# Performance work log

Measured on AMD Instinct MI355X. Metric: run time of the kernel, lower is better.

## Reference

```python
import jax, jax.numpy as jnp
import numpy as np

N_NODES = 50000
N_EDGES = 800000
F_IN = 128
HID = 32
H_IN = 4
N_CLS = 47
H_OUT = 4
NEG_SLOPE = 0.2


def _param(k, shape, scale=0.1):
    return jax.random.normal(k, shape, dtype=jnp.float32) * scale


def setup_inputs() -> dict:
    key = jax.random.key(0)
    ks = jax.random.split(key, 14)
    return {
        "x": jax.random.normal(ks[0], (N_NODES, F_IN), dtype=jnp.float32),
        "edge_index": jax.random.randint(ks[1], (2, N_EDGES), 0, N_NODES, dtype=jnp.int64),
        # layer 1: in -> hidden, heads_in, concat
        "W1": _param(ks[2], (F_IN, H_IN * HID)),
        "a1s": _param(ks[3], (H_IN, HID)),
        "a1d": _param(ks[4], (H_IN, HID)),
        "b1": _param(ks[5], (H_IN * HID,)),
        # layer 2: hidden*heads -> hidden, heads_in, concat
        "W2": _param(ks[6], (H_IN * HID, H_IN * HID)),
        "a2s": _param(ks[7], (H_IN, HID)),
        "a2d": _param(ks[8], (H_IN, HID)),
        "b2": _param(ks[9], (H_IN * HID,)),
        # layer 3: hidden*heads -> out, heads_out, mean (concat=False)
        "W3": _param(ks[10], (H_IN * HID, H_OUT * N_CLS)),
        "a3s": _param(ks[11], (H_OUT, N_CLS)),
        "a3d": _param(ks[12], (H_OUT, N_CLS)),
        "b3": _param(ks[13], (N_CLS,)),
    }


def gat_conv(x, W, att_src, att_dst, bias, src, dst, concat):
    """PyG GATConv (self-loops pre-appended in src/dst, eval mode)."""
    n = x.shape[0]
    H, C = att_src.shape
    h = (x @ W).reshape(n, H, C)                      # [N, H, C]
    a_src = jnp.sum(h * att_src[None], axis=-1)       # [N, H]
    a_dst = jnp.sum(h * att_dst[None], axis=-1)       # [N, H]
    alpha = a_src[src] + a_dst[dst]                   # [E, H]
    alpha = jnp.where(alpha >= 0, alpha, NEG_SLOPE * alpha)
    # segment softmax over destination nodes
    m = jax.ops.segment_max(alpha, dst, num_segments=n)  # [N, H]
    e = jnp.exp(alpha - m[dst])
    denom = jax.ops.segment_sum(e, dst, num_segments=n)  # [N, H]
    w = e / denom[dst]                                   # [E, H]
    msg = h[src] * w[:, :, None]                         # [E, H, C]
    out = jax.ops.segment_sum(msg, dst, num_segments=n)  # [N, H, C]
    if concat:
        out = out.reshape(n, H * C)
    else:
        out = out.mean(axis=1)
    return out + bias


def reference(x, edge_index, W1, a1s, a1d, b1, W2, a2s, a2d, b2, W3, a3s, a3d, b3):
    n = x.shape[0]
    loops = jnp.arange(n, dtype=edge_index.dtype)
    src = jnp.concatenate([edge_index[0], loops])
    dst = jnp.concatenate([edge_index[1], loops])
    h = gat_conv(x, W1, a1s, a1d, b1, src, dst, concat=True)
    h = jax.nn.relu(h)
    h = gat_conv(h, W2, a2s, a2d, b2, src, dst, concat=True)
    h = jax.nn.relu(h)
    h = gat_conv(h, W3, a3s, a3d, b3, src, dst, concat=False)
    return jax.nn.log_softmax(h, axis=1)
```

## Files before the change

### kernel.cpp

```cpp
#include <hip/hip_runtime.h>

typedef unsigned short u16;
typedef unsigned int uint32;
typedef __attribute__((ext_vector_type(8))) short short8;
typedef __attribute__((ext_vector_type(4))) float float4v;

#define N_NODES 50000
#define N_EDGES 800000
#define N_TOT   850000
#define SCAN_BLOCKS ((N_NODES + 255) / 256)
#define NBH 256
#define NB_BKT ((N_NODES + 255) >> 8)

__device__ __forceinline__ float b2f(u16 u) {
  return __uint_as_float(((unsigned int)u) << 16);
}
__device__ __forceinline__ u16 f2b(float f) {
  unsigned int x = __float_as_uint(f);
  unsigned int r = (x + 0x7fffu + ((x >> 16) & 1u)) >> 16;
  return (u16)r;
}
__device__ __forceinline__ float lo_bf(uint32 g) { return __uint_as_float(g << 16); }
__device__ __forceinline__ float hi_bf(uint32 g) { return __uint_as_float(g & 0xffff0000u); }
__device__ __forceinline__ u16 conv_elem(const void* src, int i, int isf32) {
  if (isf32) return f2b(((const float*)src)[i]);
  return ((const u16*)src)[i];
}
__device__ __forceinline__ float lrelu(float a) { return (a >= 0.f) ? a : 0.2f * a; }
__device__ __forceinline__ int eget(const int* __restrict__ ei, int i, int isI64) {
  return isI64 ? ei[2 * i] : ei[i];
}

__global__ void detect_mode(const u16* __restrict__ x16, const int* __restrict__ ei32,
                            int* __restrict__ flags) {
  __shared__ int sh_f32, sh_i32;
  int tid = threadIdx.x;
  if (tid == 0) { sh_f32 = 0; sh_i32 = 0; }
  __syncthreads();
  int emax = 0;
  for (int i = tid; i < 4096; i += 256) {
    int e = (x16[i] >> 7) & 0xFF;
    emax = emax > e ? emax : e;
  }
  if (emax >= 140) atomicOr(&sh_f32, 1);
  if (ei32[2 * tid + 1] != 0) atomicOr(&sh_i32, 1);
  __syncthreads();
  if (tid == 0) { flags[0] = sh_f32; flags[1] = sh_i32 ? 0 : 1; }
}

__global__ void convert_x4(const void* __restrict__ x, const int* __restrict__ flags,
                           u16* __restrict__ out, int n4) {
  int i = blockIdx.x * blockDim.x + threadIdx.x;
  if (i >= n4) return;
  if (flags[0]) {
    float4 v = ((const float4*)x)[i];
    ushort4 o;
    o.x = f2b(v.x); o.y = f2b(v.y); o.z = f2b(v.z); o.w = f2b(v.w);
    ((ushort4*)out)[i] = o;
  } else {
    ((ushort4*)out)[i] = ((const ushort4*)x)[i];
  }
}

__global__ void reorder_all(const void* W1, const void* W2, const void* W3,
                            const void* a1s, const void* a1d, const void* b1,
                            const void* a2s, const void* a2d, const void* b2,
                            const void* a3s, const void* a3d, const void* b3,
                            const int* __restrict__ flags,
                            u16* __restrict__ Wf1, u16* __restrict__ Wf2,
                            u16* __restrict__ Wf3, u16* __restrict__ wt) {
  int idx = blockIdx.x * blockDim.x + threadIdx.x;
  int f32 = flags[0];
  if (idx < 57344) {
    const void* W; u16* Wf; int NCOLS, li;
    if (idx < 16384)      { W = W1; Wf = Wf1; NCOLS = 128; li = idx; }
    else if (idx < 32768) { W = W2; Wf = Wf2; NCOLS = 128; li = idx - 16384; }
    else                  { W = W3; Wf = Wf3; NCOLS = 188; li = idx - 32768; }
    int j = li & 7;
    int l = (li >> 3) & 63;
    int c = (li >> 9) & 3;
    int t = li >> 11;
    int k = c * 32 + (l >> 4) * 8 + j;
    int n = t * 16 + (l & 15);
    Wf[li] = (n < NCOLS) ? conv_elem(W, k * NCOLS + n, f32) : (u16)0;
  } else {
    int li = idx - 57344;
    const void* src; int off;
    if (li < 128)       { src = a1s; off = 16384; }
    else if (li < 256)  { src = a1d; off = 16512; li -= 128; }
    else if (li < 384)  { src = b1;  off = 16640; li -= 256; }
    else if (li < 512)  { src = a2s; off = 33152; li -= 384; }
    else if (li < 640)  { src = a2d; off = 33280; li -= 512; }
    else if (li < 768)  { src = b2;  off = 33408; li -= 640; }
    else if (li < 956)  { src = a3s; off = 57600; li -= 768; }
    else if (li < 1144) { src = a3d; off = 57788; li -= 956; }
    else if (li < 1191) { src = b3;  off = 57976; li -= 1144; }
    else return;
    wt[off + li] = conv_elem(src, li, f32);
  }
}


__global__ __launch_bounds__(256) void pack_hist(const int* __restrict__ ei,
                                                 const int* __restrict__ flags,
                                                 uint32* __restrict__ epack,
                                                 int* __restrict__ cnt, int nE) {
  __shared__ int hist[NB_BKT];
  for (int t = threadIdx.x; t < NB_BKT; t += 256) hist[t] = 0;
  __syncthreads();
  const int i64 = flags[1];
  const int chunk = (nE + NBH - 1) / NBH;
  const int lo = blockIdx.x * chunk;
  const int hi = min(lo + chunk, nE);
  for (int e = lo + (int)threadIdx.x; e < hi; e += 256) {
    int s = eget(ei, e, i64);
    int d = eget(ei, nE + e, i64);
    epack[e] = ((uint32)d << 16) | (uint32)s;
    atomicAdd(&hist[d >> 8], 1);
  }
  __syncthreads();
  for (int t = threadIdx.x; t < NB_BKT; t += 256) cnt[t * NBH + blockIdx.x] = hist[t];
}

__global__ __launch_bounds__(256) void scan_cols(int* __restrict__ cnt,
                                                 int* __restrict__ total) {
  __shared__ int ws[4];
  const int bkt = blockIdx.x;
  const int tid = threadIdx.x, lane = tid & 63, wv = tid >> 6;
  int v = cnt[bkt * NBH + tid];
  int incl = v;
#pragma unroll
  for (int off = 1; off < 64; off <<= 1) {
    int t = __shfl_up(incl, off, 64);
    if (lane >= off) incl += t;
  }
  if (lane == 63) ws[wv] = incl;
  __syncthreads();
  if (tid == 0) {
    int s = 0;
#pragma unroll
    for (int w = 0; w < 4; w++) { int t = ws[w]; ws[w] = s; s += t; }
    total[bkt] = s;
  }
  __syncthreads();
  cnt[bkt * NBH + tid] = ws[wv] + incl - v;
}

__global__ __launch_bounds__(256) void scan_base(const int* __restrict__ total,
                                                 int* __restrict__ base) {
  __shared__ int ws[4];
  const int tid = threadIdx.x, lane = tid & 63, wv = tid >> 6;
  int v = (tid < NB_BKT) ? total[tid] : 0;
  int incl = v;
#pragma unroll
  for (int off = 1; off < 64; off <<= 1) {
    int t = __shfl_up(incl, off, 64);
    if (lane >= off) incl += t;
  }
  if (lane == 63) ws[wv] = incl;
  __syncthreads();
  if (tid == 0) {
    int s = 0;
#pragma unroll
    for (int w = 0; w < 4; w++) { int t = ws[w]; ws[w] = s; s += t; }
    base[NB_BKT] = s;
  }
  __syncthreads();
  if (tid < NB_BKT) base[tid] = ws[wv] + incl - v;
}

__global__ __launch_bounds__(256) void scatter_coarse(const uint32* __restrict__ epack,
                                                      const int* __restrict__ cnt,
                                                      const int* __restrict__ base,
                                                      uint32* __restrict__ staging, int nE) {
  __shared__ int lcur[NB_BKT];
  for (int t = threadIdx.x; t < NB_BKT; t += 256)
    lcur[t] = base[t] + cnt[t * NBH + blockIdx.x];
  __syncthreads();
  const int chunk = (nE + NBH - 1) / NBH;
  const int lo = blockIdx.x * chunk;
  const int hi = min(lo + chunk, nE);
  for (int e = lo + (int)threadIdx.x; e < hi; e += 256) {
    uint32 pk = epack[e];
    int p = atomicAdd(&lcur[pk >> 24], 1);
    staging[p] = pk;
  }
}

__global__ __launch_bounds__(256) void bucket_deg(const uint32* __restrict__ staging,
                                                  const int* __restrict__ base,
                                                  int* __restrict__ deg, int nN) {
  __shared__ int hist[256];
  const int b = blockIdx.x;
  hist[threadIdx.x] = 0;
  __syncthreads();
  const int lo = base[b], hi = base[b + 1];
  for (int i = lo + (int)threadIdx.x; i < hi; i += 256)
    atomicAdd(&hist[(staging[i] >> 16) & 255], 1);
  __syncthreads();
  const int n = (b << 8) + threadIdx.x;
  if (n < nN) deg[n] = hist[threadIdx.x];
}

__global__ __launch_bounds__(256) void scan_blocks(const int* __restrict__ deg,
                                                   int* __restrict__ part,
                                                   int* __restrict__ bsum, int n) {
  __shared__ int ws[4];
  int tid = threadIdx.x;
  int gid = blockIdx.x * 256 + tid;
  int lane = tid & 63, wv = tid >> 6;
  int v = (gid < n) ? (deg[gid] + 1) : 0;
  int incl = v;
#pragma unroll
  for (int off = 1; off < 64; off <<= 1) {
    int t = __shfl_up(incl, off, 64);
    if (lane >= off) incl += t;
  }
  if (lane == 63) ws[wv] = incl;
  __syncthreads();
  if (tid == 0) {
    int s = 0;
#pragma unroll
    for (int w = 0; w < 4; w++) { int t = ws[w]; ws[w] = s; s += t; }
    bsum[blockIdx.x] = s;
  }
  __syncthreads();
  if (gid < n) part[gid] = ws[wv] + incl - v;
}

__global__ __launch_bounds__(256) void scan_bsum(const int* __restrict__ bsum,
                                                 int* __restrict__ boff,
                                                 int* __restrict__ total, int nb) {
  __shared__ int ws[4];
  int tid = threadIdx.x;
  int lane = tid & 63, wv = tid >> 6;
  int v = (tid < nb) ? bsum[tid] : 0;
  int incl = v;
#pragma unroll
  for (int off = 1; off < 64; off <<= 1) {
    int t = __shfl_up(incl, off, 64);
    if (lane >= off) incl += t;
  }
  if (lane == 63) ws[wv] = incl;
  __syncthreads();
  if (tid == 0) {
    int s = 0;
#pragma unroll
    for (int w = 0; w < 4; w++) { int t = ws[w]; ws[w] = s; s += t; }
    *total = s;
  }
  __syncthreads();
  if (tid < nb) boff[tid] = ws[wv] + incl - v;
}

__global__ __launch_bounds__(256) void scan_add(int* __restrict__ row_start,
                                                const int* __restrict__ boff,
                                                const int* __restrict__ deg,
                                                u16* __restrict__ csr_dst,
                                                u16* __restrict__ csr_src,
                                                int* __restrict__ csr_src32, int n) {
  int gid = blockIdx.x * 256 + threadIdx.x;
  if (gid < n) {
    int v = row_start[gid] + boff[blockIdx.x];
    row_start[gid] = v;
    csr_src[v] = (u16)gid;
    csr_src32[v] = gid;
    int cnt = deg[gid] + 1;
    u16 g16 = (u16)gid;
    for (int k = 0; k < cnt; k++) csr_dst[v + k] = g16;
  }
}

__global__ __launch_bounds__(256) void place_csr(const uint32* __restrict__ staging,
                                                 const int* __restrict__ base,
                                                 const int* __restrict__ row_start,
                                                 u16* __restrict__ csr_src16,
                                                 int* __restrict__ csr_src32, int nN) {
  __shared__ int cur[256];
  const int b = blockIdx.x;
  const int n = (b << 8) + threadIdx.x;
  if (n < nN) cur[threadIdx.x] = row_start[n] + 1;
  __syncthreads();
  const int lo = base[b], hi = base[b + 1];
  for (int i = lo + (int)threadIdx.x; i < hi; i += 256) {
    uint32 pk = staging[i];
    int p = atomicAdd(&cur[(pk >> 16) & 255], 1);
    u16 s = (u16)(pk & 0xffffu);
    csr_src16[p] = s;
    csr_src32[p] = (int)s;
  }
}

template <int NT, int NCOLS, int STRIDE, bool FUSE_A, bool CMAJOR, bool FUSE3>
__global__ __launch_bounds__(256) void gemm_mfma(const u16* __restrict__ X,
                                                 const u16* __restrict__ Wf,
                                                 const u16* __restrict__ attS,
                                                 const u16* __restrict__ attD,
                                                 u16* __restrict__ H,
                                                 float* __restrict__ a_s,
                                                 float* __restrict__ a_d, int M) {
  const int wid = __builtin_amdgcn_readfirstlane(threadIdx.x >> 6);
  const int lane = threadIdx.x & 63;
  const int row0 = (blockIdx.x * 4 + wid) * 16;
  if (row0 >= M) return;
  const int qr = lane >> 4;
  const int ln = lane & 15;

  float4v acc[NT];
#pragma unroll
  for (int t = 0; t < NT; t++) acc[t] = (float4v){0.f, 0.f, 0.f, 0.f};

  const short8* Wf8 = (const short8*)Wf;
  const u16* xrow = X + (size_t)(row0 + ln) * 128 + qr * 8;

#pragma unroll
  for (int c = 0; c < 4; c++) {
    short8 afrag = *(const short8*)(xrow + c * 32);
#pragma unroll
    for (int t = 0; t < NT; t++) {
      short8 bfrag = Wf8[(t * 4 + c) * 64 + lane];
      acc[t] = __builtin_amdgcn_mfma_f32_16x16x32_bf16(afrag, bfrag, acc[t], 0, 0, 0);
    }
  }

#pragma unroll
  for (int t = 0; t < NT; t++) {
    int col = t * 16 + ln;
    if (col < NCOLS) {
      int off;
      if constexpr (CMAJOR) {
        int h = (col >= 141) ? 3 : (col >= 94) ? 2 : (col >= 47) ? 1 : 0;
        int c = col - h * 47;
        off = c * 4 + h;
      } else {
        off = col;
      }
#pragma unroll
      for (int i = 0; i < 4; i++) {
        H[(size_t)(row0 + qr * 4 + i) * STRIDE + off] = f2b(acc[t][i]);
      }
    }
  }

  if constexpr (FUSE_A) {
    float aSf[NT], aDf[NT];
#pragma unroll
    for (int t = 0; t < NT; t++) {
      aSf[t] = b2f(attS[t * 16 + ln]);
      aDf[t] = b2f(attD[t * 16 + ln]);
    }
#pragma unroll
    for (int h = 0; h < 4; h++) {
#pragma unroll
      for (int i = 0; i < 4; i++) {
        float s = acc[2 * h][i] * aSf[2 * h] + acc[2 * h + 1][i] * aSf[2 * h + 1];
        float d = acc[2 * h][i] * aDf[2 * h] + acc[2 * h + 1][i] * aDf[2 * h + 1];
#pragma unroll
        for (int m = 1; m < 16; m <<= 1) {
          s += __shfl_xor(s, m, 64);
          d += __shfl_xor(d, m, 64);
        }
        if (ln == 0) {
          int r = row0 + qr * 4 + i;
          a_s[r * 4 + h] = s;
          a_d[r * 4 + h] = d;
        }
      }
    }
  }

  if constexpr (FUSE3) {
    float sh[4][4], dh[4][4];
#pragma unroll
    for (int h = 0; h < 4; h++)
#pragma unroll
      for (int i = 0; i < 4; i++) { sh[h][i] = 0.f; dh[h][i] = 0.f; }
#pragma unroll
    for (int t = 0; t < NT; t++) {
      int col = t * 16 + ln;
      bool v = (col < NCOLS);
      float aS = v ? b2f(attS[col]) : 0.f;
      float aD = v ? b2f(attD[col]) : 0.f;
      int hh = (col >= 141) ? 3 : (col >= 94) ? 2 : (col >= 47) ? 1 : 0;
      float aS0 = (hh == 0) ? aS : 0.f, aS1 = (hh == 1) ? aS : 0.f;
      float aS2 = (hh == 2) ? aS : 0.f, aS3 = (hh == 3) ? aS : 0.f;
      float aD0 = (hh == 0) ? aD : 0.f, aD1 = (hh == 1) ? aD : 0.f;
      float aD2 = (hh == 2) ? aD : 0.f, aD3 = (hh == 3) ? aD : 0.f;
#pragma unroll
      for (int i = 0; i < 4; i++) {
        float a = acc[t][i];
        sh[0][i] += a * aS0; sh[1][i] += a * aS1;
        sh[2][i] += a * aS2; sh[3][i] += a * aS3;
        dh[0][i] += a * aD0; dh[1][i] += a * aD1;
        dh[2][i] += a * aD2; dh[3][i] += a * aD3;
      }
    }
#pragma unroll
    for (int h = 0; h < 4; h++) {
#pragma unroll
      for (int i = 0; i < 4; i++) {
        float s = sh[h][i], d = dh[h][i];
#pragma unroll
        for (int m = 1; m < 16; m <<= 1) {
          s += __shfl_xor(s, m, 64);
          d += __shfl_xor(d, m, 64);
        }
        if (ln == 0) {
          int r = row0 + qr * 4 + i;
          a_s[r * 4 + h] = s;
          a_d[r * 4 + h] = d;
        }
      }
    }
  }
}

__global__ __launch_bounds__(256) void edge_weights(const u16* __restrict__ csr_src,
                                                    const u16* __restrict__ csr_dst,
                                                    const float* __restrict__ a_s,
                                                    const float* __restrict__ a_d,
                                                    uint2* __restrict__ w, int nE) {
  int e = blockIdx.x * blockDim.x + threadIdx.x;
  if (e >= nE) return;
  int s = csr_src[e], d = csr_dst[e];
  float4 as = ((const float4*)a_s)[s];
  float4 ad = ((const float4*)a_d)[d];
  float w0 = __expf(lrelu(as.x + ad.x));
  float w1 = __expf(lrelu(as.y + ad.y));
  float w2 = __expf(lrelu(as.z + ad.z));
  float w3 = __expf(lrelu(as.w + ad.w));
  uint2 o;
  o.x = ((uint32)f2b(w1) << 16) | (uint32)f2b(w0);
  o.y = ((uint32)f2b(w3) << 16) | (uint32)f2b(w2);
  w[e] = o;
}


__global__ __launch_bounds__(256) void aggregate12(const u16* __restrict__ h,
                                                   const u16* __restrict__ wbuf,
                                                   const int* __restrict__ row_start,
                                                   const int* __restrict__ csr_src,
                                                   const u16* __restrict__ bias,
                                                   u16* __restrict__ out, int nN) {
  const int lane = threadIdx.x & 63;
  const int wid = __builtin_amdgcn_readfirstlane(threadIdx.x >> 6);
  const int n = blockIdx.x * 4 + wid;
  if (n >= nN) return;
  const int hL = lane >> 4;
  const uint32* h32 = (const uint32*)h;
  const float bias0 = b2f(bias[2 * lane]);
  const float bias1 = b2f(bias[2 * lane + 1]);
  int beg = row_start[n], end = row_start[n + 1];

  float acc0 = 0.f, acc1 = 0.f, den = 0.f;
  int e = beg;
  for (; e + 3 < end; e += 4) {
    int s[4];
    u16 wv[4];
    uint32 g[4];
#pragma unroll
    for (int j = 0; j < 4; j++) s[j] = csr_src[e + j];
#pragma unroll
    for (int j = 0; j < 4; j++) wv[j] = wbuf[(e + j) * 4 + hL];
#pragma unroll
    for (int j = 0; j < 4; j++) g[j] = h32[s[j] * 64 + lane];
#pragma unroll
    for (int j = 0; j < 4; j++) {
      float w = b2f(wv[j]);
      den += w;
      acc0 += w * lo_bf(g[j]);
      acc1 += w * hi_bf(g[j]);
    }
  }
  for (; e < end; ++e) {
    int s = csr_src[e];
    float w = b2f(wbuf[e * 4 + hL]);
    uint32 g = h32[s * 64 + lane];
    den += w;
    acc0 += w * lo_bf(g);
    acc1 += w * hi_bf(g);
  }
  float inv = 1.0f / den;
  float o0 = fmaxf(acc0 * inv + bias0, 0.f);
  float o1 = fmaxf(acc1 * inv + bias1, 0.f);
  uint32 packed = ((uint32)f2b(o1) << 16) | (uint32)f2b(o0);
  ((uint32*)out)[n * 64 + lane] = packed;
}

__global__ __launch_bounds__(256) void aggregate3(const u16* __restrict__ h3,
                                                  const uint2* __restrict__ wbuf,
                                                  const int* __restrict__ row_start,
                                                  const int* __restrict__ csr_src,
                                                  const u16* __restrict__ b3,
                                                  const int* __restrict__ flags,
                                                  void* __restrict__ out, int nN) {
  const int lane = threadIdx.x & 63;
  const int wid = __builtin_amdgcn_readfirstlane(threadIdx.x >> 6);
  const int n = blockIdx.x * 4 + wid;
  if (n >= nN) return;
  const bool act = lane < 47;
  const int lidx = act ? lane : 0;
  const float b3v = act ? b2f(b3[lane]) : 0.f;
  const int isf32 = flags[0];
  const uint2* h3v = (const uint2*)h3;
  int beg = row_start[n], end = row_start[n + 1];

  float den0 = 0.f, den1 = 0.f, den2 = 0.f, den3 = 0.f;
  float acc0 = 0.f, acc1 = 0.f, acc2 = 0.f, acc3 = 0.f;
  int e = beg;
  for (; e + 3 < end; e += 4) {
    int s[4];
    uint2 wp[4];
    uint2 g[4];
#pragma unroll
    for (int j = 0; j < 4; j++) s[j] = csr_src[e + j];
#pragma unroll
    for (int j = 0; j < 4; j++) wp[j] = wbuf[e + j];
#pragma unroll
    for (int j = 0; j < 4; j++) g[j] = h3v[(size_t)s[j] * 48 + lidx];
#pragma unroll
    for (int j = 0; j < 4; j++) {
      float w0 = lo_bf(wp[j].x), w1 = hi_bf(wp[j].x);
      float w2 = lo_bf(wp[j].y), w3 = hi_bf(wp[j].y);
      den0 += w0; den1 += w1; den2 += w2; den3 += w3;
      acc0 += w0 * lo_bf(g[j].x);
      acc1 += w1 * hi_bf(g[j].x);
      acc2 += w2 * lo_bf(g[j].y);
      acc3 += w3 * hi_bf(g[j].y);
    }
  }
  for (; e < end; ++e) {
    int s = csr_src[e];
    uint2 wp = wbuf[e];
    uint2 g = h3v[(size_t)s * 48 + lidx];
    float w0 = lo_bf(wp.x), w1 = hi_bf(wp.x);
    float w2 = lo_bf(wp.y), w3 = hi_bf(wp.y);
    den0 += w0; den1 += w1; den2 += w2; den3 += w3;
    acc0 += w0 * lo_bf(g.x);
    acc1 += w1 * hi_bf(g.x);
    acc2 += w2 * lo_bf(g.y);
    acc3 += w3 * hi_bf(g.y);
  }
  float val = act ? 0.25f * (acc0 / den0 + acc1 / den1 + acc2 / den2 + acc3 / den3) + b3v
                  : -1e30f;
  float mx = val;
#pragma unroll
  for (int m = 1; m < 64; m <<= 1) mx = fmaxf(mx, __shfl_xor(mx, m, 64));
  float ex = act ? __expf(val - mx) : 0.f;
  float sm = ex;
#pragma unroll
  for (int m = 1; m < 64; m <<= 1) sm += __shfl_xor(sm, m, 64);
  float lse = mx + __logf(sm);
  if (act) {
    float r = val - lse;
    if (isf32) ((float*)out)[n * 47 + lane] = r;
    else       ((u16*)out)[n * 47 + lane] = f2b(r);
  }
}


extern "C" void kernel_launch(void* const* d_in, const int* in_sizes, int n_in,
                              void* d_out, int out_size, void* d_ws, size_t ws_size,
                              hipStream_t stream) {
  const void* x   = d_in[0];
  const void* ei  = d_in[1];
  const void* W1  = d_in[2];
  const void* a1s = d_in[3];
  const void* a1d = d_in[4];
  const void* b1  = d_in[5];
  const void* W2  = d_in[6];
  const void* a2s = d_in[7];
  const void* a2d = d_in[8];
  const void* b2  = d_in[9];
  const void* W3  = d_in[10];
  const void* a3s = d_in[11];
  const void* a3d = d_in[12];
  const void* b3  = d_in[13];
  const int* ei32 = (const int*)ei;

  auto au = [](size_t v) { return (v + 255) & ~(size_t)255; };
  char* p = (char*)d_ws;
  int* flags     = (int*)p; p += 256;
  u16* wt        = (u16*)p; p += au((size_t)58023 * 2);
  u16* Wf1       = (u16*)p; p += au((size_t)16384 * 2);
  u16* Wf2       = (u16*)p; p += au((size_t)16384 * 2);
  u16* Wf3       = (u16*)p; p += au((size_t)24576 * 2);
  int* deg       = (int*)p; p += au((size_t)N_NODES * 4);
  int* row_start = (int*)p; p += au((size_t)(N_NODES + 1) * 4);
  int* cnt       = (int*)p; p += au((size_t)NB_BKT * NBH * 4);
  int* btotal    = (int*)p; p += au((size_t)NB_BKT * 4);
  int* bbase     = (int*)p; p += au((size_t)(NB_BKT + 1) * 4);
  int* bsum      = (int*)p; p += au((size_t)SCAN_BLOCKS * 4);
  int* boff      = (int*)p; p += au((size_t)SCAN_BLOCKS * 4);
  u16* csr_src16 = (u16*)p; p += au((size_t)N_TOT * 2);
  u16* csr_dst   = (u16*)p; p += au((size_t)N_TOT * 2);
  int* csr_src32 = (int*)p; p += au((size_t)N_TOT * 4);
  uint2* wbuf    = (uint2*)p; p += au((size_t)N_TOT * 8);
  float* a_s     = (float*)p; p += au((size_t)N_NODES * 4 * 4);
  float* a_d     = (float*)p; p += au((size_t)N_NODES * 4 * 4);
  u16* x_c       = (u16*)p; p += au((size_t)N_NODES * 128 * 2);
  u16* hA        = (u16*)p; p += au((size_t)N_NODES * 128 * 2);
  u16* h3        = (u16*)p; p += au((size_t)N_NODES * 192 * 2);
  u16* hB        = x_c;
  uint32* epack   = (uint32*)h3;
  uint32* staging = (uint32*)(h3 + 1600000);

  const u16* a1sc = wt + 16384;
  const u16* a1dc = wt + 16512;
  const u16* b1c  = wt + 16640;
  const u16* a2sc = wt + 33152;
  const u16* a2dc = wt + 33280;
  const u16* b2c  = wt + 33408;
  const u16* a3sc = wt + 57600;
  const u16* a3dc = wt + 57788;
  const u16* b3c  = wt + 57976;

  const int nodeBlocks = (N_NODES + 3) / 4;
  const int gemmBlocks = (N_NODES / 16 + 3) / 4;
  const int edgeBlocks = (N_TOT + 255) / 256;

  detect_mode<<<1, 256, 0, stream>>>((const u16*)x, ei32, flags);
  convert_x4<<<(N_NODES * 128 / 4 + 255) / 256, 256, 0, stream>>>(x, flags, x_c,
                                                                  N_NODES * 128 / 4);
  reorder_all<<<229, 256, 0, stream>>>(W1, W2, W3, a1s, a1d, b1, a2s, a2d, b2,
                                       a3s, a3d, b3, flags, Wf1, Wf2, Wf3, wt);

  pack_hist<<<NBH, 256, 0, stream>>>(ei32, flags, epack, cnt, N_EDGES);
  scan_cols<<<NB_BKT, 256, 0, stream>>>(cnt, btotal);
  scan_base<<<1, 256, 0, stream>>>(btotal, bbase);
  scatter_coarse<<<NBH, 256, 0, stream>>>(epack, cnt, bbase, staging, N_EDGES);
  bucket_deg<<<NB_BKT, 256, 0, stream>>>(staging, bbase, deg, N_NODES);
  scan_blocks<<<SCAN_BLOCKS, 256, 0, stream>>>(deg, row_start, bsum, N_NODES);
  scan_bsum<<<1, 256, 0, stream>>>(bsum, boff, &row_start[N_NODES], SCAN_BLOCKS);
  scan_add<<<SCAN_BLOCKS, 256, 0, stream>>>(row_start, boff, deg, csr_dst,
                                            csr_src16, csr_src32, N_NODES);
  place_csr<<<NB_BKT, 256, 0, stream>>>(staging, bbase, row_start, csr_src16,
                                        csr_src32, N_NODES);

  gemm_mfma<8, 128, 128, true, false, false><<<gemmBlocks, 256, 0, stream>>>(
      x_c, Wf1, a1sc, a1dc, hA, a_s, a_d, N_NODES);
  edge_weights<<<edgeBlocks, 256, 0, stream>>>(csr_src16, csr_dst, a_s, a_d, wbuf, N_TOT);
  aggregate12<<<nodeBlocks, 256, 0, stream>>>(hA, (const u16*)wbuf, row_start, csr_src32,
                                              b1c, hB, N_NODES);

  gemm_mfma<8, 128, 128, true, false, false><<<gemmBlocks, 256, 0, stream>>>(
      hB, Wf2, a2sc, a2dc, hA, a_s, a_d, N_NODES);
  edge_weights<<<edgeBlocks, 256, 0, stream>>>(csr_src16, csr_dst, a_s, a_d, wbuf, N_TOT);
  aggregate12<<<nodeBlocks, 256, 0, stream>>>(hA, (const u16*)wbuf, row_start, csr_src32,
                                              b2c, hB, N_NODES);

  gemm_mfma<12, 188, 192, false, true, true><<<gemmBlocks, 256, 0, stream>>>(
      hB, Wf3, a3sc, a3dc, h3, a_s, a_d, N_NODES);
  edge_weights<<<edgeBlocks, 256, 0, stream>>>(csr_src16, csr_dst, a_s, a_d, wbuf, N_TOT);
  aggregate3<<<nodeBlocks, 256, 0, stream>>>(h3, wbuf, row_start, csr_src32, b3c, flags,
                                             d_out, N_NODES);
}
```

Measured before the change: 343.8 us.

## Use head-major feature layout for layers 1-2 and fuse CSR build kernels

Layer 1 and 2 hidden features and edge weights are stored head-major, so each aggregation block handles one head over a 32-column slab. Each wavefront processes 8 edges in parallel per step, with 8 lanes per edge, and reduces across lanes with shuffles at the end. The intent is that each head's gather working set is smaller and more cache-friendly. The four CSR-construction kernels (degree, two scans, placement) are merged into one per-bucket kernel that computes row starts from the bucket base, which removes launches and intermediate buffers. Layer 3 aggregation gains an 8-edge unrolled loop. In exchange, the head-major path launches four times as many aggregation blocks and adds shuffle reductions.

```diff
diff --git a/kernel.cpp b/kernel.cpp
--- a/kernel.cpp
+++ b/kernel.cpp
@@ -8,9 +8,9 @@
 #define N_NODES 50000
 #define N_EDGES 800000
 #define N_TOT   850000
-#define SCAN_BLOCKS ((N_NODES + 255) / 256)
 #define NBH 256
 #define NB_BKT ((N_NODES + 255) >> 8)
+#define NODE_BLOCKS ((N_NODES + 3) / 4)
 
 __device__ __forceinline__ float b2f(u16 u) {
   return __uint_as_float(((unsigned int)u) << 16);
@@ -187,29 +187,25 @@
   }
 }
 
-__global__ __launch_bounds__(256) void bucket_deg(const uint32* __restrict__ staging,
-                                                  const int* __restrict__ base,
-                                                  int* __restrict__ deg, int nN) {
+__global__ __launch_bounds__(256) void build_csr(const uint32* __restrict__ staging,
+                                                 const int* __restrict__ base,
+                                                 int* __restrict__ row_start,
+                                                 u16* __restrict__ csr_dst,
+                                                 u16* __restrict__ csr_src16,
+                                                 int* __restrict__ csr_src32, int nN) {
   __shared__ int hist[256];
+  __shared__ int cur[256];
+  __shared__ int ws[4];
   const int b = blockIdx.x;
-  hist[threadIdx.x] = 0;
+  const int tid = threadIdx.x;
+  const int lane = tid & 63, wv = tid >> 6;
+  hist[tid] = 0;
   __syncthreads();
   const int lo = base[b], hi = base[b + 1];
-  for (int i = lo + (int)threadIdx.x; i < hi; i += 256)
+  for (int i = lo + tid; i < hi; i += 256)
     atomicAdd(&hist[(staging[i] >> 16) & 255], 1);
   __syncthreads();
-  const int n = (b << 8) + threadIdx.x;
-  if (n < nN) deg[n] = hist[threadIdx.x];
-}
-
-__global__ __launch_bounds__(256) void scan_blocks(const int* __restrict__ deg,
-                                                   int* __restrict__ part,
-                                                   int* __restrict__ bsum, int n) {
-  __shared__ int ws[4];
-  int tid = threadIdx.x;
-  int gid = blockIdx.x * 256 + tid;
-  int lane = tid & 63, wv = tid >> 6;
-  int v = (gid < n) ? (deg[gid] + 1) : 0;
+  int v = hist[tid];
   int incl = v;
 #pragma unroll
   for (int off = 1; off < 64; off <<= 1) {
@@ -222,67 +218,22 @@
     int s = 0;
 #pragma unroll
     for (int w = 0; w < 4; w++) { int t = ws[w]; ws[w] = s; s += t; }
-    bsum[blockIdx.x] = s;
-  }
-  __syncthreads();
-  if (gid < n) part[gid] = ws[wv] + incl - v;
-}
-
-__global__ __launch_bounds__(256) void scan_bsum(const int* __restrict__ bsum,
-                                                 int* __restrict__ boff,
-                                                 int* __restrict__ total, int nb) {
-  __shared__ int ws[4];
-  int tid = threadIdx.x;
-  int lane = tid & 63, wv = tid >> 6;
-  int v = (tid < nb) ? bsum[tid] : 0;
-  int incl = v;
-#pragma unroll
-  for (int off = 1; off < 64; off <<= 1) {
-    int t = __shfl_up(incl, off, 64);
-    if (lane >= off) incl += t;
-  }
-  if (lane == 63) ws[wv] = incl;
-  __syncthreads();
-  if (tid == 0) {
-    int s = 0;
-#pragma unroll
-    for (int w = 0; w < 4; w++) { int t = ws[w]; ws[w] = s; s += t; }
-    *total = s;
-  }
-  __syncthreads();
-  if (tid < nb) boff[tid] = ws[wv] + incl - v;
-}
-
-__global__ __launch_bounds__(256) void scan_add(int* __restrict__ row_start,
-                                                const int* __restrict__ boff,
-                                                const int* __restrict__ deg,
-                                                u16* __restrict__ csr_dst,
-                                                u16* __restrict__ csr_src,
-                                                int* __restrict__ csr_src32, int n) {
-  int gid = blockIdx.x * 256 + threadIdx.x;
-  if (gid < n) {
-    int v = row_start[gid] + boff[blockIdx.x];
-    row_start[gid] = v;
-    csr_src[v] = (u16)gid;
-    csr_src32[v] = gid;
-    int cnt = deg[gid] + 1;
-    u16 g16 = (u16)gid;
-    for (int k = 0; k < cnt; k++) csr_dst[v + k] = g16;
-  }
-}
-
-__global__ __launch_bounds__(256) void place_csr(const uint32* __restrict__ staging,
-                                                 const int* __restrict__ base,
-                                                 const int* __restrict__ row_start,
-                                                 u16* __restrict__ csr_src16,
-                                                 int* __restrict__ csr_src32, int nN) {
-  __shared__ int cur[256];
-  const int b = blockIdx.x;
-  const int n = (b << 8) + threadIdx.x;
-  if (n < nN) cur[threadIdx.x] = row_start[n] + 1;
-  __syncthreads();
-  const int lo = base[b], hi = base[b + 1];
-  for (int i = lo + (int)threadIdx.x; i < hi; i += 256) {
+  }
+  __syncthreads();
+  int excl = ws[wv] + incl - v;
+  const int n = (b << 8) + tid;
+  if (n < nN) {
+    int rs = lo + (b << 8) + excl + tid;
+    row_start[n] = rs;
+    csr_src16[rs] = (u16)n;
+    csr_src32[rs] = n;
+    u16 g16 = (u16)n;
+    for (int k = 0; k <= v; k++) csr_dst[rs + k] = g16;
+    cur[tid] = rs + 1;
+  }
+  if (b == NB_BKT - 1 && tid == 0) row_start[nN] = N_TOT;
+  __syncthreads();
+  for (int i = lo + tid; i < hi; i += 256) {
     uint32 pk = staging[i];
     int p = atomicAdd(&cur[(pk >> 16) & 255], 1);
     u16 s = (u16)(pk & 0xffffu);
@@ -291,7 +242,8 @@
   }
 }
 
-template <int NT, int NCOLS, int STRIDE, bool FUSE_A, bool CMAJOR, bool FUSE3>
+template <int NT, int NCOLS, int STRIDE, bool FUSE_A, bool CMAJOR, bool FUSE3,
+          bool AHEAD, bool HHEAD>
 __global__ __launch_bounds__(256) void gemm_mfma(const u16* __restrict__ X,
                                                  const u16* __restrict__ Wf,
                                                  const u16* __restrict__ attS,
@@ -311,11 +263,13 @@
   for (int t = 0; t < NT; t++) acc[t] = (float4v){0.f, 0.f, 0.f, 0.f};
 
   const short8* Wf8 = (const short8*)Wf;
-  const u16* xrow = X + (size_t)(row0 + ln) * 128 + qr * 8;
+  const u16* xrow = AHEAD ? X + (size_t)(row0 + ln) * 32 + qr * 8
+                          : X + (size_t)(row0 + ln) * 128 + qr * 8;
 
 #pragma unroll
   for (int c = 0; c < 4; c++) {
-    short8 afrag = *(const short8*)(xrow + c * 32);
+    const u16* ap = AHEAD ? xrow + (size_t)c * (N_NODES * 32) : xrow + c * 32;
+    short8 afrag = *(const short8*)ap;
 #pragma unroll
     for (int t = 0; t < NT; t++) {
       short8 bfrag = Wf8[(t * 4 + c) * 64 + lane];
@@ -337,7 +291,12 @@
       }
 #pragma unroll
       for (int i = 0; i < 4; i++) {
-        H[(size_t)(row0 + qr * 4 + i) * STRIDE + off] = f2b(acc[t][i]);
+        int row = row0 + qr * 4 + i;
+        if constexpr (HHEAD) {
+          H[((size_t)(t >> 1) * N_NODES + row) * 32 + (t & 1) * 16 + ln] = f2b(acc[t][i]);
+        } else {
+          H[(size_t)row * STRIDE + off] = f2b(acc[t][i]);
+        }
       }
     }
   }
@@ -415,76 +374,95 @@
   }
 }
 
+template <bool HM>
 __global__ __launch_bounds__(256) void edge_weights(const u16* __restrict__ csr_src,
                                                     const u16* __restrict__ csr_dst,
                                                     const float* __restrict__ a_s,
                                                     const float* __restrict__ a_d,
-                                                    uint2* __restrict__ w, int nE) {
+                                                    u16* __restrict__ wout, int nE) {
   int e = blockIdx.x * blockDim.x + threadIdx.x;
   if (e >= nE) return;
   int s = csr_src[e], d = csr_dst[e];
   float4 as = ((const float4*)a_s)[s];
   float4 ad = ((const float4*)a_d)[d];
-  float w0 = __expf(lrelu(as.x + ad.x));
-  float w1 = __expf(lrelu(as.y + ad.y));
-  float w2 = __expf(lrelu(as.z + ad.z));
-  float w3 = __expf(lrelu(as.w + ad.w));
-  uint2 o;
-  o.x = ((uint32)f2b(w1) << 16) | (uint32)f2b(w0);
-  o.y = ((uint32)f2b(w3) << 16) | (uint32)f2b(w2);
-  w[e] = o;
-}
-
-
-__global__ __launch_bounds__(256) void aggregate12(const u16* __restrict__ h,
-                                                   const u16* __restrict__ wbuf,
-                                                   const int* __restrict__ row_start,
-                                                   const int* __restrict__ csr_src,
-                                                   const u16* __restrict__ bias,
-                                                   u16* __restrict__ out, int nN) {
+  float ww0 = __expf(lrelu(as.x + ad.x));
+  float ww1 = __expf(lrelu(as.y + ad.y));
+  float ww2 = __expf(lrelu(as.z + ad.z));
+  float ww3 = __expf(lrelu(as.w + ad.w));
+  if constexpr (HM) {
+    wout[e] = f2b(ww0);
+    wout[N_TOT + e] = f2b(ww1);
+    wout[2 * N_TOT + e] = f2b(ww2);
+    wout[3 * N_TOT + e] = f2b(ww3);
+  } else {
+    uint2 o;
+    o.x = ((uint32)f2b(ww1) << 16) | (uint32)f2b(ww0);
+    o.y = ((uint32)f2b(ww3) << 16) | (uint32)f2b(ww2);
+    ((uint2*)wout)[e] = o;
+  }
+}
+
+
+__global__ __launch_bounds__(256) void aggregate12_hm(const u16* __restrict__ hH,
+                                                      const u16* __restrict__ wH,
+                                                      const int* __restrict__ row_start,
+                                                      const int* __restrict__ csr_src,
+                                                      const u16* __restrict__ bias,
+                                                      u16* __restrict__ out, int nN) {
   const int lane = threadIdx.x & 63;
   const int wid = __builtin_amdgcn_readfirstlane(threadIdx.x >> 6);
-  const int n = blockIdx.x * 4 + wid;
+  const int head = __builtin_amdgcn_readfirstlane(blockIdx.x / NODE_BLOCKS);
+  const int nb = blockIdx.x - head * NODE_BLOCKS;
+  const int n = nb * 4 + wid;
   if (n >= nN) return;
-  const int hL = lane >> 4;
-  const uint32* h32 = (const uint32*)h;
-  const float bias0 = b2f(bias[2 * lane]);
-  const float bias1 = b2f(bias[2 * lane + 1]);
+  const int es = lane >> 3;
+  const int cl = lane & 7;
+  const uint2* hslab = (const uint2*)(hH + (size_t)head * (N_NODES * 32));
+  const u16* wslab = wH + (size_t)head * N_TOT;
   int beg = row_start[n], end = row_start[n + 1];
 
-  float acc0 = 0.f, acc1 = 0.f, den = 0.f;
-  int e = beg;
-  for (; e + 3 < end; e += 4) {
-    int s[4];
-    u16 wv[4];
-    uint32 g[4];
-#pragma unroll
-    for (int j = 0; j < 4; j++) s[j] = csr_src[e + j];
-#pragma unroll
-    for (int j = 0; j < 4; j++) wv[j] = wbuf[(e + j) * 4 + hL];
-#pragma unroll
-    for (int j = 0; j < 4; j++) g[j] = h32[s[j] * 64 + lane];
-#pragma unroll
-    for (int j = 0; j < 4; j++) {
-      float w = b2f(wv[j]);
-      den += w;
-      acc0 += w * lo_bf(g[j]);
-      acc1 += w * hi_bf(g[j]);
-    }
-  }
-  for (; e < end; ++e) {
-    int s = csr_src[e];
-    float w = b2f(wbuf[e * 4 + hL]);
-    uint32 g = h32[s * 64 + lane];
-    den += w;
-    acc0 += w * lo_bf(g);
-    acc1 += w * hi_bf(g);
-  }
-  float inv = 1.0f / den;
-  float o0 = fmaxf(acc0 * inv + bias0, 0.f);
-  float o1 = fmaxf(acc1 * inv + bias1, 0.f);
-  uint32 packed = ((uint32)f2b(o1) << 16) | (uint32)f2b(o0);
-  ((uint32*)out)[n * 64 + lane] = packed;
+  float acc0 = 0.f, acc1 = 0.f, acc2 = 0.f, acc3 = 0.f, den = 0.f;
+  for (int e = beg; e < end; e += 16) {
+    int i0 = e + es, i1 = e + 8 + es;
+    bool v0 = i0 < end, v1 = i1 < end;
+    int j0 = v0 ? i0 : beg;
+    int j1 = v1 ? i1 : beg;
+    int s0 = csr_src[j0];
+    int s1 = csr_src[j1];
+    float w0 = v0 ? b2f(wslab[j0]) : 0.f;
+    float w1 = v1 ? b2f(wslab[j1]) : 0.f;
+    uint2 g0 = hslab[s0 * 8 + cl];
+    uint2 g1 = hslab[s1 * 8 + cl];
+    den += w0;
+    acc0 += w0 * lo_bf(g0.x); acc1 += w0 * hi_bf(g0.x);
+    acc2 += w0 * lo_bf(g0.y); acc3 += w0 * hi_bf(g0.y);
+    den += w1;
+    acc0 += w1 * lo_bf(g1.x); acc1 += w1 * hi_bf(g1.x);
+    acc2 += w1 * lo_bf(g1.y); acc3 += w1 * hi_bf(g1.y);
+  }
+#pragma unroll
+  for (int m = 8; m < 64; m <<= 1) {
+    acc0 += __shfl_xor(acc0, m, 64);
+    acc1 += __shfl_xor(acc1, m, 64);
+    acc2 += __shfl_xor(acc2, m, 64);
+    acc3 += __shfl_xor(acc3, m, 64);
+    den += __shfl_xor(den, m, 64);
+  }
+  if (es == 0) {
+    float inv = 1.0f / den;
+    float b0 = b2f(bias[head * 32 + 4 * cl]);
+    float b1 = b2f(bias[head * 32 + 4 * cl + 1]);
+    float b2v = b2f(bias[head * 32 + 4 * cl + 2]);
+    float b3v = b2f(bias[head * 32 + 4 * cl + 3]);
+    float o0 = fmaxf(acc0 * inv + b0, 0.f);
+    float o1 = fmaxf(acc1 * inv + b1, 0.f);
+    float o2 = fmaxf(acc2 * inv + b2v, 0.f);
+    float o3 = fmaxf(acc3 * inv + b3v, 0.f);
+    uint2 pk;
+    pk.x = ((uint32)f2b(o1) << 16) | (uint32)f2b(o0);
+    pk.y = ((uint32)f2b(o3) << 16) | (uint32)f2b(o2);
+    ((uint2*)out)[(size_t)(head * N_NODES + n) * 8 + cl] = pk;
+  }
 }
 
 __global__ __launch_bounds__(256) void aggregate3(const u16* __restrict__ h3,
@@ -508,6 +486,27 @@
   float den0 = 0.f, den1 = 0.f, den2 = 0.f, den3 = 0.f;
   float acc0 = 0.f, acc1 = 0.f, acc2 = 0.f, acc3 = 0.f;
   int e = beg;
+  for (; e + 7 < end; e += 8) {
+    int s[8];
+    uint2 wp[8];
+    uint2 g[8];
+#pragma unroll
+    for (int j = 0; j < 8; j++) s[j] = csr_src[e + j];
+#pragma unroll
+    for (int j = 0; j < 8; j++) wp[j] = wbuf[e + j];
+#pragma unroll
+    for (int j = 0; j < 8; j++) g[j] = h3v[(size_t)s[j] * 48 + lidx];
+#pragma unroll
+    for (int j = 0; j < 8; j++) {
+      float w0 = lo_bf(wp[j].x), w1 = hi_bf(wp[j].x);
+      float w2 = lo_bf(wp[j].y), w3 = hi_bf(wp[j].y);
+      den0 += w0; den1 += w1; den2 += w2; den3 += w3;
+      acc0 += w0 * lo_bf(g[j].x);
+      acc1 += w1 * hi_bf(g[j].x);
+      acc2 += w2 * lo_bf(g[j].y);
+      acc3 += w3 * hi_bf(g[j].y);
+    }
+  }
   for (; e + 3 < end; e += 4) {
     int s[4];
     uint2 wp[4];
@@ -585,17 +584,14 @@
   u16* Wf1       = (u16*)p; p += au((size_t)16384 * 2);
   u16* Wf2       = (u16*)p; p += au((size_t)16384 * 2);
   u16* Wf3       = (u16*)p; p += au((size_t)24576 * 2);
-  int* deg       = (int*)p; p += au((size_t)N_NODES * 4);
   int* row_start = (int*)p; p += au((size_t)(N_NODES + 1) * 4);
   int* cnt       = (int*)p; p += au((size_t)NB_BKT * NBH * 4);
   int* btotal    = (int*)p; p += au((size_t)NB_BKT * 4);
   int* bbase     = (int*)p; p += au((size_t)(NB_BKT + 1) * 4);
-  int* bsum      = (int*)p; p += au((size_t)SCAN_BLOCKS * 4);
-  int* boff      = (int*)p; p += au((size_t)SCAN_BLOCKS * 4);
   u16* csr_src16 = (u16*)p; p += au((size_t)N_TOT * 2);
   u16* csr_dst   = (u16*)p; p += au((size_t)N_TOT * 2);
   int* csr_src32 = (int*)p; p += au((size_t)N_TOT * 4);
-  uint2* wbuf    = (uint2*)p; p += au((size_t)N_TOT * 8);
+  u16* wbuf      = (u16*)p; p += au((size_t)N_TOT * 8);
   float* a_s     = (float*)p; p += au((size_t)N_NODES * 4 * 4);
   float* a_d     = (float*)p; p += au((size_t)N_NODES * 4 * 4);
   u16* x_c       = (u16*)p; p += au((size_t)N_NODES * 128 * 2);
@@ -615,7 +611,6 @@
   const u16* a3dc = wt + 57788;
   const u16* b3c  = wt + 57976;
 
-  const int nodeBlocks = (N_NODES + 3) / 4;
   const int gemmBlocks = (N_NODES / 16 + 3) / 4;
   const int edgeBlocks = (N_TOT + 255) / 256;
 
@@ -629,29 +624,27 @@
   scan_cols<<<NB_BKT, 256, 0, stream>>>(cnt, btotal);
   scan_base<<<1, 256, 0, stream>>>(btotal, bbase);
   scatter_coarse<<<NBH, 256, 0, stream>>>(epack, cnt, bbase, staging, N_EDGES);
-  bucket_deg<<<NB_BKT, 256, 0, stream>>>(staging, bbase, deg, N_NODES);
-  scan_blocks<<<SCAN_BLOCKS, 256, 0, stream>>>(deg, row_start, bsum, N_NODES);
-  scan_bsum<<<1, 256, 0, stream>>>(bsum, boff, &row_start[N_NODES], SCAN_BLOCKS);
-  scan_add<<<SCAN_BLOCKS, 256, 0, stream>>>(row_start, boff, deg, csr_dst,
-                                            csr_src16, csr_src32, N_NODES);
-  place_csr<<<NB_BKT, 256, 0, stream>>>(staging, bbase, row_start, csr_src16,
-                                        csr_src32, N_NODES);
-
-  gemm_mfma<8, 128, 128, true, false, false><<<gemmBlocks, 256, 0, stream>>>(
+  build_csr<<<NB_BKT, 256, 0, stream>>>(staging, bbase, row_start, csr_dst,
+                                        csr_src16, csr_src32, N_NODES);
+
+  gemm_mfma<8, 128, 128, true, false, false, false, true><<<gemmBlocks, 256, 0, stream>>>(
       x_c, Wf1, a1sc, a1dc, hA, a_s, a_d, N_NODES);
-  edge_weights<<<edgeBlocks, 256, 0, stream>>>(csr_src16, csr_dst, a_s, a_d, wbuf, N_TOT);
-  aggregate12<<<nodeBlocks, 256, 0, stream>>>(hA, (const u16*)wbuf, row_start, csr_src32,
-                                              b1c, hB, N_NODES);
-
-  gemm_mfma<8, 128, 128, true, false, false><<<gemmBlocks, 256, 0, stream>>>(
+  edge_weights<true><<<edgeBlocks, 256, 0, stream>>>(csr_src16, csr_dst, a_s, a_d,
+                                                     wbuf, N_TOT);
+  aggregate12_hm<<<4 * NODE_BLOCKS, 256, 0, stream>>>(hA, wbuf, row_start, csr_src32,
+                                                      b1c, hB, N_NODES);
+
+  gemm_mfma<8, 128, 128, true, false, false, true, true><<<gemmBlocks, 256, 0, stream>>>(
       hB, Wf2, a2sc, a2dc, hA, a_s, a_d, N_NODES);
-  edge_weights<<<edgeBlocks, 256, 0, stream>>>(csr_src16, csr_dst, a_s, a_d, wbuf, N_TOT);
-  aggregate12<<<nodeBlocks, 256, 0, stream>>>(hA, (const u16*)wbuf, row_start, csr_src32,
-                                              b2c, hB, N_NODES);
-
-  gemm_mfma<12, 188, 192, false, true, true><<<gemmBlocks, 256, 0, stream>>>(
+  edge_weights<true><<<edgeBlocks, 256, 0, stream>>>(csr_src16, csr_dst, a_s, a_d,
+                                                     wbuf, N_TOT);
+  aggregate12_hm<<<4 * NODE_BLOCKS, 256, 0, stream>>>(hA, wbuf, row_start, csr_src32,
+                                                      b2c, hB, N_NODES);
+
+  gemm_mfma<12, 188, 192, false, true, true, true, false><<<gemmBlocks, 256, 0, stream>>>(
       hB, Wf3, a3sc, a3dc, h3, a_s, a_d, N_NODES);
-  edge_weights<<<edgeBlocks, 256, 0, stream>>>(csr_src16, csr_dst, a_s, a_d, wbuf, N_TOT);
-  aggregate3<<<nodeBlocks, 256, 0, stream>>>(h3, wbuf, row_start, csr_src32, b3c, flags,
-                                             d_out, N_NODES);
-}
+  edge_weights<false><<<edgeBlocks, 256, 0, stream>>>(csr_src16, csr_dst, a_s, a_d,
+                                                      wbuf, N_TOT);
+  aggregate3<<<NODE_BLOCKS, 256, 0, stream>>>(h3, (const uint2*)wbuf, row_start,
+                                              csr_src32, b3c, flags, d_out, N_NODES);
+}
```

Measured after the change: 408.0 us. 18.7% more time.

## Fuse CSR build kernels and compute edge weights inline in layer 1-2 aggregation

Applied to the files above, without the earlier changes.

The separate degree histogram, three scan kernels and placement kernel are merged into one per-bucket build_csr kernel. It derives row offsets from the bucket base plus a local scan, which removes four launches and the deg/bsum/boff buffers. Layers 1 and 2 no longer launch edge_weights; aggregate12 gathers a_s per source and recomputes exp(lrelu) inline, which drops the write and read of the per-edge weight buffer in exchange for an extra gather and exp per edge per lane. aggregate3 also gains an 8-way unrolled edge loop for more memory-level parallelism.

```diff
diff --git a/kernel.cpp b/kernel.cpp
--- a/kernel.cpp
+++ b/kernel.cpp
@@ -8,9 +8,9 @@
 #define N_NODES 50000
 #define N_EDGES 800000
 #define N_TOT   850000
-#define SCAN_BLOCKS ((N_NODES + 255) / 256)
 #define NBH 256
 #define NB_BKT ((N_NODES + 255) >> 8)
+#define NODE_BLOCKS ((N_NODES + 3) / 4)
 
 __device__ __forceinline__ float b2f(u16 u) {
   return __uint_as_float(((unsigned int)u) << 16);
@@ -187,29 +187,25 @@
   }
 }
 
-__global__ __launch_bounds__(256) void bucket_deg(const uint32* __restrict__ staging,
-                                                  const int* __restrict__ base,
-                                                  int* __restrict__ deg, int nN) {
+__global__ __launch_bounds__(256) void build_csr(const uint32* __restrict__ staging,
+                                                 const int* __restrict__ base,
+                                                 int* __restrict__ row_start,
+                                                 u16* __restrict__ csr_dst,
+                                                 u16* __restrict__ csr_src16,
+                                                 int* __restrict__ csr_src32, int nN) {
   __shared__ int hist[256];
+  __shared__ int cur[256];
+  __shared__ int ws[4];
   const int b = blockIdx.x;
-  hist[threadIdx.x] = 0;
+  const int tid = threadIdx.x;
+  const int lane = tid & 63, wv = tid >> 6;
+  hist[tid] = 0;
   __syncthreads();
   const int lo = base[b], hi = base[b + 1];
-  for (int i = lo + (int)threadIdx.x; i < hi; i += 256)
+  for (int i = lo + tid; i < hi; i += 256)
     atomicAdd(&hist[(staging[i] >> 16) & 255], 1);
   __syncthreads();
-  const int n = (b << 8) + threadIdx.x;
-  if (n < nN) deg[n] = hist[threadIdx.x];
-}
-
-__global__ __launch_bounds__(256) void scan_blocks(const int* __restrict__ deg,
-                                                   int* __restrict__ part,
-                                                   int* __restrict__ bsum, int n) {
-  __shared__ int ws[4];
-  int tid = threadIdx.x;
-  int gid = blockIdx.x * 256 + tid;
-  int lane = tid & 63, wv = tid >> 6;
-  int v = (gid < n) ? (deg[gid] + 1) : 0;
+  int v = hist[tid];
   int incl = v;
 #pragma unroll
   for (int off = 1; off < 64; off <<= 1) {
@@ -222,67 +218,22 @@
     int s = 0;
 #pragma unroll
     for (int w = 0; w < 4; w++) { int t = ws[w]; ws[w] = s; s += t; }
-    bsum[blockIdx.x] = s;
-  }
-  __syncthreads();
-  if (gid < n) part[gid] = ws[wv] + incl - v;
-}
-
-__global__ __launch_bounds__(256) void scan_bsum(const int* __restrict__ bsum,
-                                                 int* __restrict__ boff,
-                                                 int* __restrict__ total, int nb) {
-  __shared__ int ws[4];
-  int tid = threadIdx.x;
-  int lane = tid & 63, wv = tid >> 6;
-  int v = (tid < nb) ? bsum[tid] : 0;
-  int incl = v;
-#pragma unroll
-  for (int off = 1; off < 64; off <<= 1) {
-    int t = __shfl_up(incl, off, 64);
-    if (lane >= off) incl += t;
-  }
-  if (lane == 63) ws[wv] = incl;
-  __syncthreads();
-  if (tid == 0) {
-    int s = 0;
-#pragma unroll
-    for (int w = 0; w < 4; w++) { int t = ws[w]; ws[w] = s; s += t; }
-    *total = s;
-  }
-  __syncthreads();
-  if (tid < nb) boff[tid] = ws[wv] + incl - v;
-}
-
-__global__ __launch_bounds__(256) void scan_add(int* __restrict__ row_start,
-                                                const int* __restrict__ boff,
-                                                const int* __restrict__ deg,
-                                                u16* __restrict__ csr_dst,
-                                                u16* __restrict__ csr_src,
-                                                int* __restrict__ csr_src32, int n) {
-  int gid = blockIdx.x * 256 + threadIdx.x;
-  if (gid < n) {
-    int v = row_start[gid] + boff[blockIdx.x];
-    row_start[gid] = v;
-    csr_src[v] = (u16)gid;
-    csr_src32[v] = gid;
-    int cnt = deg[gid] + 1;
-    u16 g16 = (u16)gid;
-    for (int k = 0; k < cnt; k++) csr_dst[v + k] = g16;
-  }
-}
-
-__global__ __launch_bounds__(256) void place_csr(const uint32* __restrict__ staging,
-                                                 const int* __restrict__ base,
-                                                 const int* __restrict__ row_start,
-                                                 u16* __restrict__ csr_src16,
-                                                 int* __restrict__ csr_src32, int nN) {
-  __shared__ int cur[256];
-  const int b = blockIdx.x;
-  const int n = (b << 8) + threadIdx.x;
-  if (n < nN) cur[threadIdx.x] = row_start[n] + 1;
-  __syncthreads();
-  const int lo = base[b], hi = base[b + 1];
-  for (int i = lo + (int)threadIdx.x; i < hi; i += 256) {
+  }
+  __syncthreads();
+  int excl = ws[wv] + incl - v;
+  const int n = (b << 8) + tid;
+  if (n < nN) {
+    int rs = lo + (b << 8) + excl + tid;
+    row_start[n] = rs;
+    csr_src16[rs] = (u16)n;
+    csr_src32[rs] = n;
+    u16 g16 = (u16)n;
+    for (int k = 0; k <= v; k++) csr_dst[rs + k] = g16;
+    cur[tid] = rs + 1;
+  }
+  if (b == NB_BKT - 1 && tid == 0) row_start[nN] = N_TOT;
+  __syncthreads();
+  for (int i = lo + tid; i < hi; i += 256) {
     uint32 pk = staging[i];
     int p = atomicAdd(&cur[(pk >> 16) & 255], 1);
     u16 s = (u16)(pk & 0xffffu);
@@ -437,7 +388,8 @@
 
 
 __global__ __launch_bounds__(256) void aggregate12(const u16* __restrict__ h,
-                                                   const u16* __restrict__ wbuf,
+                                                   const float* __restrict__ a_s,
+                                                   const float* __restrict__ a_d,
                                                    const int* __restrict__ row_start,
                                                    const int* __restrict__ csr_src,
                                                    const u16* __restrict__ bias,
@@ -450,23 +402,24 @@
   const uint32* h32 = (const uint32*)h;
   const float bias0 = b2f(bias[2 * lane]);
   const float bias1 = b2f(bias[2 * lane + 1]);
+  const float adv = a_d[n * 4 + hL];
   int beg = row_start[n], end = row_start[n + 1];
 
   float acc0 = 0.f, acc1 = 0.f, den = 0.f;
   int e = beg;
   for (; e + 3 < end; e += 4) {
     int s[4];
-    u16 wv[4];
+    float av[4];
     uint32 g[4];
 #pragma unroll
     for (int j = 0; j < 4; j++) s[j] = csr_src[e + j];
 #pragma unroll
-    for (int j = 0; j < 4; j++) wv[j] = wbuf[(e + j) * 4 + hL];
+    for (int j = 0; j < 4; j++) av[j] = a_s[s[j] * 4 + hL];
 #pragma unroll
     for (int j = 0; j < 4; j++) g[j] = h32[s[j] * 64 + lane];
 #pragma unroll
     for (int j = 0; j < 4; j++) {
-      float w = b2f(wv[j]);
+      float w = __expf(lrelu(av[j] + adv));
       den += w;
       acc0 += w * lo_bf(g[j]);
       acc1 += w * hi_bf(g[j]);
@@ -474,7 +427,7 @@
   }
   for (; e < end; ++e) {
     int s = csr_src[e];
-    float w = b2f(wbuf[e * 4 + hL]);
+    float w = __expf(lrelu(a_s[s * 4 + hL] + adv));
     uint32 g = h32[s * 64 + lane];
     den += w;
     acc0 += w * lo_bf(g);
@@ -508,6 +461,27 @@
   float den0 = 0.f, den1 = 0.f, den2 = 0.f, den3 = 0.f;
   float acc0 = 0.f, acc1 = 0.f, acc2 = 0.f, acc3 = 0.f;
   int e = beg;
+  for (; e + 7 < end; e += 8) {
+    int s[8];
+    uint2 wp[8];
+    uint2 g[8];
+#pragma unroll
+    for (int j = 0; j < 8; j++) s[j] = csr_src[e + j];
+#pragma unroll
+    for (int j = 0; j < 8; j++) wp[j] = wbuf[e + j];
+#pragma unroll
+    for (int j = 0; j < 8; j++) g[j] = h3v[(size_t)s[j] * 48 + lidx];
+#pragma unroll
+    for (int j = 0; j < 8; j++) {
+      float w0 = lo_bf(wp[j].x), w1 = hi_bf(wp[j].x);
+      float w2 = lo_bf(wp[j].y), w3 = hi_bf(wp[j].y);
+      den0 += w0; den1 += w1; den2 += w2; den3 += w3;
+      acc0 += w0 * lo_bf(g[j].x);
+      acc1 += w1 * hi_bf(g[j].x);
+      acc2 += w2 * lo_bf(g[j].y);
+      acc3 += w3 * hi_bf(g[j].y);
+    }
+  }
   for (; e + 3 < end; e += 4) {
     int s[4];
     uint2 wp[4];
@@ -585,13 +559,10 @@
   u16* Wf1       = (u16*)p; p += au((size_t)16384 * 2);
   u16* Wf2       = (u16*)p; p += au((size_t)16384 * 2);
   u16* Wf3       = (u16*)p; p += au((size_t)24576 * 2);
-  int* deg       = (int*)p; p += au((size_t)N_NODES * 4);
   int* row_start = (int*)p; p += au((size_t)(N_NODES + 1) * 4);
   int* cnt       = (int*)p; p += au((size_t)NB_BKT * NBH * 4);
   int* btotal    = (int*)p; p += au((size_t)NB_BKT * 4);
   int* bbase     = (int*)p; p += au((size_t)(NB_BKT + 1) * 4);
-  int* bsum      = (int*)p; p += au((size_t)SCAN_BLOCKS * 4);
-  int* boff      = (int*)p; p += au((size_t)SCAN_BLOCKS * 4);
   u16* csr_src16 = (u16*)p; p += au((size_t)N_TOT * 2);
   u16* csr_dst   = (u16*)p; p += au((size_t)N_TOT * 2);
   int* csr_src32 = (int*)p; p += au((size_t)N_TOT * 4);
@@ -615,7 +586,6 @@
   const u16* a3dc = wt + 57788;
   const u16* b3c  = wt + 57976;
 
-  const int nodeBlocks = (N_NODES + 3) / 4;
   const int gemmBlocks = (N_NODES / 16 + 3) / 4;
   const int edgeBlocks = (N_TOT + 255) / 256;
 
@@ -629,29 +599,22 @@
   scan_cols<<<NB_BKT, 256, 0, stream>>>(cnt, btotal);
   scan_base<<<1, 256, 0, stream>>>(btotal, bbase);
   scatter_coarse<<<NBH, 256, 0, stream>>>(epack, cnt, bbase, staging, N_EDGES);
-  bucket_deg<<<NB_BKT, 256, 0, stream>>>(staging, bbase, deg, N_NODES);
-  scan_blocks<<<SCAN_BLOCKS, 256, 0, stream>>>(deg, row_start, bsum, N_NODES);
-  scan_bsum<<<1, 256, 0, stream>>>(bsum, boff, &row_start[N_NODES], SCAN_BLOCKS);
-  scan_add<<<SCAN_BLOCKS, 256, 0, stream>>>(row_start, boff, deg, csr_dst,
-                                            csr_src16, csr_src32, N_NODES);
-  place_csr<<<NB_BKT, 256, 0, stream>>>(staging, bbase, row_start, csr_src16,
-                                        csr_src32, N_NODES);
+  build_csr<<<NB_BKT, 256, 0, stream>>>(staging, bbase, row_start, csr_dst,
+                                        csr_src16, csr_src32, N_NODES);
 
   gemm_mfma<8, 128, 128, true, false, false><<<gemmBlocks, 256, 0, stream>>>(
       x_c, Wf1, a1sc, a1dc, hA, a_s, a_d, N_NODES);
-  edge_weights<<<edgeBlocks, 256, 0, stream>>>(csr_src16, csr_dst, a_s, a_d, wbuf, N_TOT);
-  aggregate12<<<nodeBlocks, 256, 0, stream>>>(hA, (const u16*)wbuf, row_start, csr_src32,
-                                              b1c, hB, N_NODES);
+  aggregate12<<<NODE_BLOCKS, 256, 0, stream>>>(hA, a_s, a_d, row_start, csr_src32,
+                                               b1c, hB, N_NODES);
 
   gemm_mfma<8, 128, 128, true, false, false><<<gemmBlocks, 256, 0, stream>>>(
       hB, Wf2, a2sc, a2dc, hA, a_s, a_d, N_NODES);
-  edge_weights<<<edgeBlocks, 256, 0, stream>>>(csr_src16, csr_dst, a_s, a_d, wbuf, N_TOT);
-  aggregate12<<<nodeBlocks, 256, 0, stream>>>(hA, (const u16*)wbuf, row_start, csr_src32,
-                                              b2c, hB, N_NODES);
+  aggregate12<<<NODE_BLOCKS, 256, 0, stream>>>(hA, a_s, a_d, row_start, csr_src32,
+                                               b2c, hB, N_NODES);
 
   gemm_mfma<12, 188, 192, false, true, true><<<gemmBlocks, 256, 0, stream>>>(
       hB, Wf3, a3sc, a3dc, h3, a_s, a_d, N_NODES);
   edge_weights<<<edgeBlocks, 256, 0, stream>>>(csr_src16, csr_dst, a_s, a_d, wbuf, N_TOT);
-  aggregate3<<<nodeBlocks, 256, 0, stream>>>(h3, wbuf, row_start, csr_src32, b3c, flags,
-                                             d_out, N_NODES);
-}
+  aggregate3<<<NODE_BLOCKS, 256, 0, stream>>>(h3, wbuf, row_start, csr_src32, b3c, flags,
+                                              d_out, N_NODES);
+}
```

Measured after the change: 323.1 us. 1.06x faster.
